# Performance work log

Measured on AMD Instinct MI355X. Metric: run time of the kernel, lower is better.

The kernel has to match this reference:

```python
import jax, jax.numpy as jnp
import numpy as np

L = 10   # lattice side (hardcoded self.length)
K = 3    # kernel_size -> half_k = 1 wrap padding
FN = 4   # filter_num
B = 262144


def setup_inputs() -> dict:
    key = jax.random.key(0)
    k1, k2, k3, k4, k5 = jax.random.split(key, 5)
    v = jax.random.normal(k1, (B, L * L), dtype=jnp.float32)
    # torch default init scale ~ 1/sqrt(fan_in)
    conv_w = jax.random.normal(k2, (FN, 1, K, K), dtype=jnp.float32) / 3.0
    conv_b = jax.random.normal(k3, (FN,), dtype=jnp.float32) * 0.1
    deconv_w = jax.random.normal(k4, (FN, 1, 2, 2), dtype=jnp.float32) / 4.0
    deconv_b = jax.random.normal(k5, (1,), dtype=jnp.float32) * 0.1
    data = jnp.zeros((1,), dtype=jnp.int32)  # unused positional arg of log_psi
    return {"v": v, "conv_w": conv_w, "conv_b": conv_b,
            "deconv_w": deconv_w, "deconv_b": deconv_b, "data": data}


def _log_psi(v, conv_w, conv_b, deconv_w, deconv_b):
    b = v.shape[0]
    x = v.reshape(b, 1, L, L)
    # handmade_padding == periodic (wrap) pad of width half_k=1 on both spatial axes
    x = jnp.pad(x, ((0, 0), (0, 0), (1, 1), (1, 1)), mode="wrap")  # [B,1,12,12]
    # Conv2d(1, FN, 3), VALID -> [B,FN,10,10]
    y = jax.lax.conv_general_dilated(
        x, conv_w, window_strides=(1, 1), padding="VALID",
        dimension_numbers=("NCHW", "OIHW", "NCHW"))
    y = y + conv_b[None, :, None, None]
    # MaxPool2d(2,2): non-overlapping 2x2 -> [B,FN,5,5]
    y = y.reshape(b, FN, L // 2, 2, L // 2, 2).max(axis=(3, 5))
    # ConvTranspose2d(FN,1,kernel=2,stride=2): each input pixel -> disjoint 2x2 block
    # torch weight layout [in=FN, out=1, 2, 2]
    z = jnp.einsum("bcij,cokl->boikjl", y, deconv_w).reshape(b, 1, L, L)
    z = z + deconv_b[None, :, None, None]
    sign_z = jnp.sign(z)
    abs_z = z * sign_z
    sign_prod = sign_z.reshape(b, -1).prod(axis=1)        # scalar per sample
    log_sum = jnp.log(abs_z).reshape(b, -1).sum(axis=1)   # scalar per sample
    return sign_prod, log_sum


def reference(v, conv_w, conv_b, deconv_w, deconv_b, data):
    return _log_psi(v, conv_w, conv_b, deconv_w, deconv_b)
```

## Files before the change

### kernel.cpp

```cpp
#include <hip/hip_runtime.h>
#include <math.h>


#define SREAD(x) __int_as_float(__builtin_amdgcn_readfirstlane(__float_as_int(x)))

__device__ __forceinline__ void load_pair(float (&P)[20], const float* base) {
    const float4* s = (const float4*)base;
    #pragma unroll
    for (int t = 0; t < 5; ++t) {
        float4 q = s[t];
        P[4 * t + 0] = q.x;
        P[4 * t + 1] = q.y;
        P[4 * t + 2] = q.z;
        P[4 * t + 3] = q.w;
    }
}

__device__ __forceinline__ void pool_row(
    const float (&pa)[20], const float (&pb)[20], const float (&pc)[20],
    const float (&W)[4][9], const float (&Cb)[4], const float (&Dw)[4][4],
    const float Db, const int j2base ,
    unsigned& sbits, float& l2)
{
    (void)j2base;
    float Xw[4][10];
    #pragma unroll
    for (int c = 0; c < 10; ++c) {
        Xw[0][c] = pa[10 + c];
        Xw[1][c] = pb[c];
        Xw[2][c] = pb[10 + c];
        Xw[3][c] = pc[c];
    }
    #pragma unroll
    for (int j = 0; j < 5; ++j) {
        float p0, p1, p2, p3;
        #pragma unroll
        for (int dr = 0; dr < 2; ++dr) {
            #pragma unroll
            for (int dc = 0; dc < 2; ++dc) {
                float a0 = Cb[0], a1 = Cb[1], a2 = Cb[2], a3 = Cb[3];
                #pragma unroll
                for (int kr = 0; kr < 3; ++kr) {
                    #pragma unroll
                    for (int kc = 0; kc < 3; ++kc) {
                        const int cc = (2 * j + dc + kc + 9) % 10;
                        const float xv = Xw[dr + kr][cc];
                        const int t = kr * 3 + kc;
                        a0 = fmaf(xv, W[0][t], a0);
                        a1 = fmaf(xv, W[1][t], a1);
                        a2 = fmaf(xv, W[2][t], a2);
                        a3 = fmaf(xv, W[3][t], a3);
                    }
                }
                if (dr == 0 && dc == 0) {
                    p0 = a0; p1 = a1; p2 = a2; p3 = a3;
                } else {
                    p0 = fmaxf(p0, a0); p1 = fmaxf(p1, a1);
                    p2 = fmaxf(p2, a2); p3 = fmaxf(p3, a3);
                }
            }
        }
        float z[4];
        #pragma unroll
        for (int kl = 0; kl < 4; ++kl) {
            float zz = Db;
            zz = fmaf(p0, Dw[0][kl], zz);
            zz = fmaf(p1, Dw[1][kl], zz);
            zz = fmaf(p2, Dw[2][kl], zz);
            zz = fmaf(p3, Dw[3][kl], zz);
            z[kl] = zz;
            sbits ^= __float_as_uint(zz);
        }
        l2 += __log2f(fabsf(z[0] * z[1])) + __log2f(fabsf(z[2] * z[3]));
    }
}

__global__ __launch_bounds__(256) void CNN2D_37495064494620_kernel(
    const float* __restrict__ v,
    const float* __restrict__ cw,
    const float* __restrict__ cb,
    const float* __restrict__ dw,
    const float* __restrict__ db,
    float* __restrict__ out,
    int B)
{
    const int b = blockIdx.x * 256 + threadIdx.x;
    if (b >= B) return;

    float W[4][9];
    #pragma unroll
    for (int f = 0; f < 4; ++f)
        #pragma unroll
        for (int t = 0; t < 9; ++t)
            W[f][t] = SREAD(cw[f * 9 + t]);
    float Cb[4];
    #pragma unroll
    for (int f = 0; f < 4; ++f) Cb[f] = SREAD(cb[f]);
    float Dw[4][4];
    #pragma unroll
    for (int f = 0; f < 4; ++f)
        #pragma unroll
        for (int t = 0; t < 4; ++t)
            Dw[f][t] = SREAD(dw[f * 4 + t]);
    const float Db = SREAD(db[0]);

    const float* src = v + (size_t)b * 100;

    unsigned sbits = 0u;
    float l2 = 0.0f;

    float P0[20], P1[20], P2[20], P3[20], P4[20], P1b[20];

    load_pair(P0, src + 0);
    load_pair(P1, src + 20);
    load_pair(P2, src + 40);
    load_pair(P3, src + 60);

    pool_row(P0, P1, P2, W, Cb, Dw, Db, 0, sbits, l2);

    load_pair(P4, src + 80);

    pool_row(P1, P2, P3, W, Cb, Dw, Db, 0, sbits, l2);

    pool_row(P2, P3, P4, W, Cb, Dw, Db, 0, sbits, l2);

    load_pair(P1b, src + 20);

    pool_row(P3, P4, P0, W, Cb, Dw, Db, 0, sbits, l2);

    pool_row(P4, P0, P1b, W, Cb, Dw, Db, 0, sbits, l2);

    out[b]     = (sbits & 0x80000000u) ? -1.0f : 1.0f;
    out[B + b] = l2 * 0.69314718055994531f;
}

extern "C" void kernel_launch(void* const* d_in, const int* in_sizes, int n_in,
                              void* d_out, int out_size, void* d_ws, size_t ws_size,
                              hipStream_t stream) {
    const float* v  = (const float*)d_in[0];
    const float* cw = (const float*)d_in[1];
    const float* cb = (const float*)d_in[2];
    const float* dw = (const float*)d_in[3];
    const float* db = (const float*)d_in[4];
    float* out = (float*)d_out;

    const int B = in_sizes[0] / 100;
    const int grid = (B + 255) / 256;
    CNN2D_37495064494620_kernel<<<grid, 256, 0, stream>>>(v, cw, cb, dw, db, out, B);
}
```

Measured before the change: 174.1 us.

## Stage input rows through LDS with coalesced global_load_lds, 64-thread blocks

Each 64-thread block now copies its 64 contiguous 100-float samples into shared memory using global_load_lds 16-byte transfers that are fully coalesced across lanes. Each thread then reads its own row from LDS instead of making strided per-thread float4 global loads. This removes the poorly coalesced global access pattern. In exchange it adds 25.6 KB of LDS per block, a barrier, likely LDS bank conflicts from the 100-float row stride, and removes the bounds check on B.

```diff
diff --git a/kernel.cpp b/kernel.cpp
--- a/kernel.cpp
+++ b/kernel.cpp
@@ -4,7 +4,14 @@
 
 #define SREAD(x) __int_as_float(__builtin_amdgcn_readfirstlane(__float_as_int(x)))
 
-__device__ __forceinline__ void load_pair(float (&P)[20], const float* base) {
+__device__ __forceinline__ void gload_lds16(const float* g, float* l) {
+    __builtin_amdgcn_global_load_lds(
+        (const __attribute__((address_space(1))) void*)g,
+        (__attribute__((address_space(3))) void*)l,
+        16, 0, 0);
+}
+
+__device__ __forceinline__ void load_pair_lds(float (&P)[20], const float* base) {
     const float4* s = (const float4*)base;
     #pragma unroll
     for (int t = 0; t < 5; ++t) {
@@ -19,10 +26,8 @@
 __device__ __forceinline__ void pool_row(
     const float (&pa)[20], const float (&pb)[20], const float (&pc)[20],
     const float (&W)[4][9], const float (&Cb)[4], const float (&Dw)[4][4],
-    const float Db, const int j2base ,
-    unsigned& sbits, float& l2)
+    const float Db, unsigned& sbits, float& l2)
 {
-    (void)j2base;
     float Xw[4][10];
     #pragma unroll
     for (int c = 0; c < 10; ++c) {
@@ -75,7 +80,7 @@
     }
 }
 
-__global__ __launch_bounds__(256) void CNN2D_37495064494620_kernel(
+__global__ __launch_bounds__(64) void CNN2D_37495064494620_kernel(
     const float* __restrict__ v,
     const float* __restrict__ cw,
     const float* __restrict__ cb,
@@ -84,8 +89,15 @@
     float* __restrict__ out,
     int B)
 {
-    const int b = blockIdx.x * 256 + threadIdx.x;
-    if (b >= B) return;
+    const int lane = threadIdx.x;
+    const int b = blockIdx.x * 64 + lane;
+
+    __shared__ __align__(16) float sm[64 * 100];
+
+    const float* wbase = v + (size_t)blockIdx.x * 64 * 100;
+    #pragma unroll
+    for (int k = 0; k < 25; ++k)
+        gload_lds16(wbase + k * 256 + lane * 4, &sm[k * 256]);
 
     float W[4][9];
     #pragma unroll
@@ -104,31 +116,33 @@
             Dw[f][t] = SREAD(dw[f * 4 + t]);
     const float Db = SREAD(db[0]);
 
-    const float* src = v + (size_t)b * 100;
+    __syncthreads();
+
+    const float* my = sm + lane * 100;
 
     unsigned sbits = 0u;
     float l2 = 0.0f;
 
     float P0[20], P1[20], P2[20], P3[20], P4[20], P1b[20];
 
-    load_pair(P0, src + 0);
-    load_pair(P1, src + 20);
-    load_pair(P2, src + 40);
-    load_pair(P3, src + 60);
+    load_pair_lds(P0, my + 0);
+    load_pair_lds(P1, my + 20);
+    load_pair_lds(P2, my + 40);
+    load_pair_lds(P3, my + 60);
 
-    pool_row(P0, P1, P2, W, Cb, Dw, Db, 0, sbits, l2);
+    pool_row(P0, P1, P2, W, Cb, Dw, Db, sbits, l2);
 
-    load_pair(P4, src + 80);
+    load_pair_lds(P4, my + 80);
 
-    pool_row(P1, P2, P3, W, Cb, Dw, Db, 0, sbits, l2);
+    pool_row(P1, P2, P3, W, Cb, Dw, Db, sbits, l2);
 
-    pool_row(P2, P3, P4, W, Cb, Dw, Db, 0, sbits, l2);
+    pool_row(P2, P3, P4, W, Cb, Dw, Db, sbits, l2);
 
-    load_pair(P1b, src + 20);
+    load_pair_lds(P1b, my + 20);
 
-    pool_row(P3, P4, P0, W, Cb, Dw, Db, 0, sbits, l2);
+    pool_row(P3, P4, P0, W, Cb, Dw, Db, sbits, l2);
 
-    pool_row(P4, P0, P1b, W, Cb, Dw, Db, 0, sbits, l2);
+    pool_row(P4, P0, P1b, W, Cb, Dw, Db, sbits, l2);
 
     out[b]     = (sbits & 0x80000000u) ? -1.0f : 1.0f;
     out[B + b] = l2 * 0.69314718055994531f;
@@ -145,6 +159,6 @@
     float* out = (float*)d_out;
 
     const int B = in_sizes[0] / 100;
-    const int grid = (B + 255) / 256;
-    CNN2D_37495064494620_kernel<<<grid, 256, 0, stream>>>(v, cw, cb, dw, db, out, B);
+    const int grid = (B + 63) / 64;
+    CNN2D_37495064494620_kernel<<<grid, 64, 0, stream>>>(v, cw, cb, dw, db, out, B);
 }
```

New measurement: 175.3 us. No clear change (+0.7%).
